# Performance work log

Measured on AMD Instinct MI355X. Metric: run time of the kernel, lower is better.

## Reference

```python
import jax, jax.numpy as jnp
import numpy as np

RADIUS = 4
SIGMA_X = 5.0
SIGMA_I = 1.0


def gaussian_kernel3d():
    # norm.pdf(d)/norm.pdf(0) == exp(-d^2/2)
    r = RADIUS
    n = 2 * r + 1
    v = np.linspace(-r, r, n) ** 2
    xy, yz, zx = np.meshgrid(v, v, v)
    dist = (xy + yz + zx) / SIGMA_X
    k = np.exp(-0.5 * dist ** 2).astype(np.float32)  # (9,9,9)
    return jnp.asarray(k)


def setup_inputs() -> dict:
    key = jax.random.key(0)
    k1, k2 = jax.random.split(key)
    B, C, K, D, H, W = 2, 1, 5, 96, 96, 96
    inputs = jax.random.normal(k1, (B, C, D, H, W), jnp.float32)
    logits = jax.random.normal(k2, (B, K, D, H, W), jnp.float32)
    labels = jax.nn.softmax(logits, axis=1)  # class probabilities
    return {"inputs": inputs, "labels": labels}


def reference(inputs, labels):
    # inputs: [B,C,D,H,W] raw image; labels: [B,K,D,H,W] class probs
    K = labels.shape[1]
    kernel = gaussian_kernel3d()
    eps_m, eps_d = 1e-5, 1e-6

    # per-class, per-channel weighted mean: [B,K,C]
    num_mean = jnp.mean(inputs[:, None] * labels[:, :, None], axis=(3, 4, 5))
    den_mean = jnp.mean(labels, axis=(2, 3, 4))[..., None] + eps_m  # [B,K,1]
    class_mean = num_mean / den_mean  # [B,K,C]

    # diff: sum over channels of (x - mean)^2 -> [B,K,D,H,W]
    diff = jnp.sum((inputs[:, None] - class_mean[..., None, None, None]) ** 2, axis=2)
    weights = jnp.exp(-(diff ** 2) / (SIGMA_I ** 2))  # [B,K,D,H,W]

    # depthwise (per-class) 3D conv with the shared Gaussian kernel
    rhs = jnp.broadcast_to(kernel[None, None], (K, 1) + kernel.shape)  # [K,1,9,9,9]
    pad = [(RADIUS, RADIUS)] * 3

    def conv(x):  # x: [B,K,D,H,W]
        return jax.lax.conv_general_dilated(
            x, rhs, window_strides=(1, 1, 1), padding=pad,
            dimension_numbers=("NCDHW", "OIDHW", "NCDHW"),
            feature_group_count=K)

    numer = jnp.sum(labels * conv(labels * weights), axis=(0, 2, 3, 4))  # [K]
    denom = jnp.sum(labels * conv(weights), axis=(0, 2, 3, 4))  # [K]
    loss = jnp.sum(jnp.abs(numer / (denom + eps_d)))  # L1Loss vs zeros per class
    return jnp.asarray(K, inputs.dtype) - loss
```

## Files before the change

kernel.cpp:

```cpp
#include <hip/hip_runtime.h>
#include <math.h>

#define VOL (96*96*96)
#define KCLS 5
#define CZ 12
#define PSTR 64
#define PROWS 40
#define PSZ (PROWS*PSTR)
#define NS2 15

typedef __attribute__((ext_vector_type(8))) short bf16x8;
typedef __attribute__((ext_vector_type(4))) float f32x4;
typedef __attribute__((ext_vector_type(4))) unsigned short us4;

constexpr int S2VALS[NS2] = {0,1,2,4,5,8,9,10,13,16,17,18,20,25,32};
constexpr int MAP33[33] = {0,1,2,-1,3,4,-1,-1,5,6,7,-1,-1,8,-1,-1,
                           9,10,11,-1,12,-1,-1,-1,-1,13,-1,-1,-1,-1,-1,-1,14};

__device__ __forceinline__ unsigned short f2bf(float f) {
  unsigned u = __builtin_bit_cast(unsigned, f);
  u += 0x7fffu + ((u >> 16) & 1u);
  return (unsigned short)(u >> 16);
}


__global__ __launch_bounds__(256) void k_sums(const float* __restrict__ I,
                                              const float* __restrict__ L,
                                              double* __restrict__ ws) {
  const int b = blockIdx.y;
  const int base = blockIdx.x * 256 + threadIdx.x;
  const float4 iv = ((const float4*)(I + b * VOL))[base];
  float sL[KCLS], sIL[KCLS];
#pragma unroll
  for (int k = 0; k < KCLS; ++k) {
    const float4 lv = ((const float4*)(L + (b * KCLS + k) * VOL))[base];
    sL[k] = (lv.x + lv.y) + (lv.z + lv.w);
    sIL[k] = iv.x * lv.x + iv.y * lv.y + iv.z * lv.z + iv.w * lv.w;
  }
#pragma unroll
  for (int k = 0; k < KCLS; ++k) {
#pragma unroll
    for (int off = 32; off; off >>= 1) {
      sL[k] += __shfl_down(sL[k], off);
      sIL[k] += __shfl_down(sIL[k], off);
    }
  }
  __shared__ double red[4][2 * KCLS];
  const int wid = threadIdx.x >> 6;
  if ((threadIdx.x & 63) == 0) {
#pragma unroll
    for (int k = 0; k < KCLS; ++k) {
      red[wid][k] = (double)sL[k];
      red[wid][KCLS + k] = (double)sIL[k];
    }
  }
  __syncthreads();
  if (threadIdx.x < 2 * KCLS) {
    double v = red[0][threadIdx.x] + red[1][threadIdx.x] + red[2][threadIdx.x] + red[3][threadIdx.x];
    const int k = threadIdx.x % KCLS;
    const int which = threadIdx.x / KCLS;
    const int slot = blockIdx.x & 31;
    atomicAdd(&ws[32 + which * 320 + (b * KCLS + k) * 32 + slot], v);
  }
}

__global__ __launch_bounds__(256, 3) void k_conv(const float* __restrict__ I,
                                                 const float* __restrict__ L,
                                                 double* __restrict__ ws) {
  __shared__ __attribute__((aligned(16))) short Wp[2][PSZ];
  __shared__ __attribute__((aligned(16))) short LWp[2][PSZ];
  __shared__ double red[8];
  __shared__ float meanS;

  const int t = threadIdx.x;
  const int vol = blockIdx.z;
  const int kcl = vol % KCLS;
  const int b = vol / KCLS;
  const int x0 = (blockIdx.x % 3) * 32;
  const int y0 = (blockIdx.x / 3) * 32;
  const int z0 = blockIdx.y * CZ;

  const float* __restrict__ Ib = I + b * VOL;
  const float* __restrict__ Lb = L + vol * VOL;

  if (t < 32) {
    double a = ws[32 + vol * 32 + t];
    double c = ws[352 + vol * 32 + t];
#pragma unroll
    for (int off = 16; off; off >>= 1) {
      a += __shfl_down(a, off);
      c += __shfl_down(c, off);
    }
    if (t == 0) meanS = (float)(c / (a + 1e-5 * (double)VOL));
  }
  __syncthreads();
  const float mean = meanS;

  const int lane = t & 63;
  const int w = t >> 6;
  const int wx = w & 1, wy = w >> 1;
  const int nn = lane & 15, qq = lane >> 4;
  const int gyOut = y0 + 16 * wy + nn;
  const int gxOut = x0 + 16 * wx + 4 * qq;

  bf16x8 afr[NS2];
#pragma unroll
  for (int r = 0; r < NS2; ++r) {
    const float s2c = (float)S2VALS[r];
    bf16x8 v;
#pragma unroll
    for (int j = 0; j < 8; ++j) {
      const int dx = 8 * qq + j - nn;
      float val = 0.f;
      if (dx >= 0 && dx <= 8) {
        const float q = s2c + (float)((dx - 4) * (dx - 4));
        val = __expf(-0.02f * q * q);
      }
      v[j] = (short)f2bf(val);
    }
    afr[r] = v;
  }

  f32x4 accW[9], accL[9];
  const f32x4 zer = {0.f, 0.f, 0.f, 0.f};
#pragma unroll
  for (int i = 0; i < 9; ++i) { accW[i] = zer; accL[i] = zer; }
  float pN = 0.f, pD = 0.f;

  auto stagePlane = [&](int buf, int zp) {
#pragma unroll
    for (int ii = 0; ii < 2; ++ii) {
      const int qi = t + ii * 256;
      if (qi < 480) {
        const int row = qi / 12;
        const int q = qi - row * 12;
        const int xq = q * 4;
        const int gy = y0 - 4 + row, gx = x0 - 4 + xq;
        const bool ok = ((unsigned)gy < 96u) && ((unsigned)gx <= 92u);
        float4 iv = make_float4(0.f, 0.f, 0.f, 0.f);
        float4 lv = make_float4(0.f, 0.f, 0.f, 0.f);
        if (ok) {
          const int off = (zp * 96 + gy) * 96 + gx;
          iv = *(const float4*)(Ib + off);
          lv = *(const float4*)(Lb + off);
        }
        float d, w0, w1, w2, w3;
        d = iv.x - mean; d = d * d; w0 = ok ? __expf(-d * d) : 0.f;
        d = iv.y - mean; d = d * d; w1 = ok ? __expf(-d * d) : 0.f;
        d = iv.z - mean; d = d * d; w2 = ok ? __expf(-d * d) : 0.f;
        d = iv.w - mean; d = d * d; w3 = ok ? __expf(-d * d) : 0.f;
        us4 wv = { f2bf(w0), f2bf(w1), f2bf(w2), f2bf(w3) };
        us4 ov = { f2bf(lv.x * w0), f2bf(lv.y * w1), f2bf(lv.z * w2), f2bf(lv.w * w3) };
        const int c = q >> 1, o = (q & 1) << 2;
        const int a = row * PSTR + (((c ^ (row & 7)) << 3) + o);
        *(us4*)(&Wp[buf][a]) = wv;
        *(us4*)(&LWp[buf][a]) = ov;
      }
    }
  };

  auto computeEdge = [&](int buf, int iLo, int iHi) {
    const short* __restrict__ Wb = Wp[buf];
    const short* __restrict__ Lwb = LWp[buf];
    const int yb = 16 * wy + nn;
    const int csel = 2 * wx + qq;
    int boff = yb * PSTR + (((csel ^ (yb & 7))) << 3);
    bf16x8 bw = *(const bf16x8*)(Wb + boff);
    bf16x8 bl = *(const bf16x8*)(Lwb + boff);
#pragma unroll
    for (int dy = 0; dy < 9; ++dy) {
      bf16x8 nbw, nbl;
      if (dy < 8) {
        const int yrow = yb + dy + 1;
        const int nboff = yrow * PSTR + (((csel ^ (yrow & 7))) << 3);
        nbw = *(const bf16x8*)(Wb + nboff);
        nbl = *(const bf16x8*)(Lwb + nboff);
      }
      const int dy2c = (dy - 4) * (dy - 4);
#pragma unroll
      for (int i = 0; i < 9; ++i) {
        if (i >= iLo && i <= iHi) {
          const int da = (i < 4) ? (4 - i) : (i - 4);
          const int ri = MAP33[dy2c + da * da];
          accW[i] = __builtin_amdgcn_mfma_f32_16x16x32_bf16(afr[ri], bw, accW[i], 0, 0, 0);
          accL[i] = __builtin_amdgcn_mfma_f32_16x16x32_bf16(afr[ri], bl, accL[i], 0, 0, 0);
        }
      }
      bw = nbw; bl = nbl;
    }
  };

  const int zp0 = z0 - 4;
  const int zend = z0 + CZ + 4;
  if ((unsigned)zp0 <= 95u) stagePlane(0, zp0);
  __syncthreads();

  for (int zp = zp0; zp < zend; ++zp) {
    const int cur = (zp - zp0) & 1;
    const int zo = zp - 4;
    const bool lok = (zo >= z0) && (zo < z0 + CZ);
    float4 lab = make_float4(0.f, 0.f, 0.f, 0.f);
    if (lok) lab = *(const float4*)(Lb + (zo * 96 + gyOut) * 96 + gxOut);

    if ((unsigned)zp <= 95u) {
      int iLo = z0 - zo; if (iLo < 0) iLo = 0;
      int iHi = (z0 + CZ - 1) - zo; if (iHi > 8) iHi = 8;
      computeEdge(cur, iLo, iHi);
    }
    if (lok) {
      pN += accL[0].x * lab.x + accL[0].y * lab.y + accL[0].z * lab.z + accL[0].w * lab.w;
      pD += accW[0].x * lab.x + accW[0].y * lab.y + accW[0].z * lab.z + accW[0].w * lab.w;
    }
#pragma unroll
    for (int i = 0; i < 8; ++i) { accW[i] = accW[i + 1]; accL[i] = accL[i + 1]; }
    accW[8] = zer; accL[8] = zer;

    const int zn = zp + 1;
    if (zn < zend && (unsigned)zn <= 95u) stagePlane(cur ^ 1, zn);
    __syncthreads();
  }

#pragma unroll
  for (int off = 32; off; off >>= 1) {
    pN += __shfl_down(pN, off);
    pD += __shfl_down(pD, off);
  }
  if (lane == 0) { red[w] = (double)pN; red[4 + w] = (double)pD; }
  __syncthreads();
  if (t == 0) {
    const int slot = (blockIdx.x + blockIdx.y) & 15;
    atomicAdd(&ws[672 + kcl * 16 + slot], red[0] + red[1] + red[2] + red[3]);
    atomicAdd(&ws[752 + kcl * 16 + slot], red[4] + red[5] + red[6] + red[7]);
  }
}

__global__ void k_final(const double* __restrict__ ws, float* __restrict__ out) {
  __shared__ double acc[KCLS];
  const int t = threadIdx.x;
  if (t < KCLS) {
    double n = 0.0, d = 0.0;
#pragma unroll
    for (int s = 0; s < 16; ++s) {
      n += ws[672 + t * 16 + s];
      d += ws[752 + t * 16 + s];
    }
    acc[t] = fabs(n / (d + 1e-6));
  }
  __syncthreads();
  if (t == 0) {
    double loss = acc[0] + acc[1] + acc[2] + acc[3] + acc[4];
    out[0] = (float)(5.0 - loss);
  }
}

extern "C" void kernel_launch(void* const* d_in, const int* in_sizes, int n_in,
                              void* d_out, int out_size, void* d_ws, size_t ws_size,
                              hipStream_t stream) {
  (void)in_sizes; (void)n_in; (void)out_size; (void)ws_size;
  const float* I = (const float*)d_in[0];
  const float* L = (const float*)d_in[1];
  double* ws = (double*)d_ws;
  float* out = (float*)d_out;

  hipMemsetAsync(d_ws, 0, 832 * sizeof(double), stream);
  k_sums<<<dim3(864, 2, 1), 256, 0, stream>>>(I, L, ws);
  k_conv<<<dim3(9, 8, 10), 256, 0, stream>>>(I, L, ws);
  k_final<<<1, 64, 0, stream>>>(ws, out);
}
```

Measured before the change: 184.4 us.

## Async LDS plane prefetch, coarsen sums kernel, fuse final reduction into conv

The conv kernel now issues global_load_lds async copies of the next raw fp32 plane into a double-buffered LDS staging area while MFMAs run on the current bf16 plane, then converts it in a separate phase. Out-of-range planes are skipped and the tail outputs are drained after the loop. The sums kernel processes four float4s per thread with a quarter of the blocks. The separate final kernel is removed, and the last conv block, detected via an atomic counter, computes the loss. LDS use rises with the raw buffers, which may lower occupancy, and there is an extra barrier per plane.

```diff
diff --git a/kernel.cpp b/kernel.cpp
--- a/kernel.cpp
+++ b/kernel.cpp
@@ -8,6 +8,7 @@
 #define PROWS 40
 #define PSZ (PROWS*PSTR)
 #define NS2 15
+#define NQ 480
 
 typedef __attribute__((ext_vector_type(8))) short bf16x8;
 typedef __attribute__((ext_vector_type(4))) float f32x4;
@@ -23,19 +24,34 @@
   return (unsigned short)(u >> 16);
 }
 
+__device__ __forceinline__ void async16(void* lds, const void* g) {
+  __builtin_amdgcn_global_load_lds(
+      (const __attribute__((address_space(1))) void*)g,
+      (__attribute__((address_space(3))) void*)lds, 16, 0, 0);
+}
+
 
 __global__ __launch_bounds__(256) void k_sums(const float* __restrict__ I,
                                               const float* __restrict__ L,
                                               double* __restrict__ ws) {
   const int b = blockIdx.y;
-  const int base = blockIdx.x * 256 + threadIdx.x;
-  const float4 iv = ((const float4*)(I + b * VOL))[base];
+  const int base = blockIdx.x * 1024 + threadIdx.x;
+  const float4* __restrict__ I4 = (const float4*)(I + b * VOL);
+  float4 iv[4];
+#pragma unroll
+  for (int j = 0; j < 4; ++j) iv[j] = I4[base + j * 256];
   float sL[KCLS], sIL[KCLS];
-#pragma unroll
+#pragma unroll 1
   for (int k = 0; k < KCLS; ++k) {
-    const float4 lv = ((const float4*)(L + (b * KCLS + k) * VOL))[base];
-    sL[k] = (lv.x + lv.y) + (lv.z + lv.w);
-    sIL[k] = iv.x * lv.x + iv.y * lv.y + iv.z * lv.z + iv.w * lv.w;
+    const float4* __restrict__ L4 = (const float4*)(L + (b * KCLS + k) * VOL);
+    float a = 0.f, c = 0.f;
+#pragma unroll
+    for (int j = 0; j < 4; ++j) {
+      const float4 lv = L4[base + j * 256];
+      a += (lv.x + lv.y) + (lv.z + lv.w);
+      c += iv[j].x * lv.x + iv[j].y * lv.y + iv[j].z * lv.z + iv[j].w * lv.w;
+    }
+    sL[k] = a; sIL[k] = c;
   }
 #pragma unroll
   for (int k = 0; k < KCLS; ++k) {
@@ -66,11 +82,15 @@
 
 __global__ __launch_bounds__(256, 3) void k_conv(const float* __restrict__ I,
                                                  const float* __restrict__ L,
-                                                 double* __restrict__ ws) {
-  __shared__ __attribute__((aligned(16))) short Wp[2][PSZ];
-  __shared__ __attribute__((aligned(16))) short LWp[2][PSZ];
+                                                 double* __restrict__ ws,
+                                                 float* __restrict__ out) {
+  __shared__ __attribute__((aligned(16))) short Wp[PSZ];
+  __shared__ __attribute__((aligned(16))) short LWp[PSZ];
+  __shared__ float4 rawI[2][NQ];
+  __shared__ float4 rawL[2][NQ];
   __shared__ double red[8];
   __shared__ float meanS;
+  __shared__ int lastS;
 
   const int t = threadIdx.x;
   const int vol = blockIdx.z;
@@ -127,23 +147,39 @@
   for (int i = 0; i < 9; ++i) { accW[i] = zer; accL[i] = zer; }
   float pN = 0.f, pD = 0.f;
 
-  auto stagePlane = [&](int buf, int zp) {
+  int qoff[2]; bool okq[2];
+#pragma unroll
+  for (int ii = 0; ii < 2; ++ii) {
+    const int qi = t + ii * 256;
+    const int row = qi / 12;
+    const int q = qi - row * 12;
+    const int gy = y0 - 4 + row, gx = x0 - 4 + q * 4;
+    okq[ii] = (qi < NQ) && ((unsigned)gy < 96u) && ((unsigned)gx <= 92u);
+    const int cy = min(max(gy, 0), 95);
+    const int cx = min(max(gx, 0), 92);
+    qoff[ii] = cy * 96 + cx;
+  }
+  const int wbase0 = t & ~63;
+  const int wbase1 = 256 + (t & ~63);
+
+  auto asyncPlane = [&](int slot, int zp) {
+    const int poff = zp * 9216;
+    async16(&rawI[slot][wbase0], Ib + poff + qoff[0]);
+    async16(&rawL[slot][wbase0], Lb + poff + qoff[0]);
+    if (t < NQ - 256) {
+      async16(&rawI[slot][wbase1], Ib + poff + qoff[1]);
+      async16(&rawL[slot][wbase1], Lb + poff + qoff[1]);
+    }
+  };
+
+  auto convertPlane = [&](int slot) {
 #pragma unroll
     for (int ii = 0; ii < 2; ++ii) {
       const int qi = t + ii * 256;
-      if (qi < 480) {
-        const int row = qi / 12;
-        const int q = qi - row * 12;
-        const int xq = q * 4;
-        const int gy = y0 - 4 + row, gx = x0 - 4 + xq;
-        const bool ok = ((unsigned)gy < 96u) && ((unsigned)gx <= 92u);
-        float4 iv = make_float4(0.f, 0.f, 0.f, 0.f);
-        float4 lv = make_float4(0.f, 0.f, 0.f, 0.f);
-        if (ok) {
-          const int off = (zp * 96 + gy) * 96 + gx;
-          iv = *(const float4*)(Ib + off);
-          lv = *(const float4*)(Lb + off);
-        }
+      if (qi < NQ) {
+        const float4 iv = rawI[slot][qi];
+        const float4 lv = rawL[slot][qi];
+        const bool ok = okq[ii];
         float d, w0, w1, w2, w3;
         d = iv.x - mean; d = d * d; w0 = ok ? __expf(-d * d) : 0.f;
         d = iv.y - mean; d = d * d; w1 = ok ? __expf(-d * d) : 0.f;
@@ -151,30 +187,30 @@
         d = iv.w - mean; d = d * d; w3 = ok ? __expf(-d * d) : 0.f;
         us4 wv = { f2bf(w0), f2bf(w1), f2bf(w2), f2bf(w3) };
         us4 ov = { f2bf(lv.x * w0), f2bf(lv.y * w1), f2bf(lv.z * w2), f2bf(lv.w * w3) };
+        const int row = qi / 12;
+        const int q = qi - row * 12;
         const int c = q >> 1, o = (q & 1) << 2;
-        const int a = row * PSTR + (((c ^ (row & 7)) << 3) + o);
-        *(us4*)(&Wp[buf][a]) = wv;
-        *(us4*)(&LWp[buf][a]) = ov;
+        const int a = row * PSTR + ((c ^ (row & 7)) << 3) + o;
+        *(us4*)(&Wp[a]) = wv;
+        *(us4*)(&LWp[a]) = ov;
       }
     }
   };
 
-  auto computeEdge = [&](int buf, int iLo, int iHi) {
-    const short* __restrict__ Wb = Wp[buf];
-    const short* __restrict__ Lwb = LWp[buf];
+  auto computeEdge = [&](int iLo, int iHi) {
     const int yb = 16 * wy + nn;
     const int csel = 2 * wx + qq;
-    int boff = yb * PSTR + (((csel ^ (yb & 7))) << 3);
-    bf16x8 bw = *(const bf16x8*)(Wb + boff);
-    bf16x8 bl = *(const bf16x8*)(Lwb + boff);
+    int boff = yb * PSTR + ((csel ^ (yb & 7)) << 3);
+    bf16x8 bw = *(const bf16x8*)(Wp + boff);
+    bf16x8 bl = *(const bf16x8*)(LWp + boff);
 #pragma unroll
     for (int dy = 0; dy < 9; ++dy) {
       bf16x8 nbw, nbl;
       if (dy < 8) {
         const int yrow = yb + dy + 1;
-        const int nboff = yrow * PSTR + (((csel ^ (yrow & 7))) << 3);
-        nbw = *(const bf16x8*)(Wb + nboff);
-        nbl = *(const bf16x8*)(Lwb + nboff);
+        const int nboff = yrow * PSTR + ((csel ^ (yrow & 7)) << 3);
+        nbw = *(const bf16x8*)(Wp + nboff);
+        nbl = *(const bf16x8*)(LWp + nboff);
       }
       const int dy2c = (dy - 4) * (dy - 4);
 #pragma unroll
@@ -190,23 +226,28 @@
     }
   };
 
-  const int zp0 = z0 - 4;
-  const int zend = z0 + CZ + 4;
-  if ((unsigned)zp0 <= 95u) stagePlane(0, zp0);
-  __syncthreads();
-
-  for (int zp = zp0; zp < zend; ++zp) {
-    const int cur = (zp - zp0) & 1;
+  const int zlo = max(z0 - 4, 0);
+  const int zhi = min(z0 + CZ + 4, 96);
+
+  asyncPlane(0, zlo);
+  __syncthreads();
+  convertPlane(0);
+  __syncthreads();
+
+  for (int zp = zlo; zp < zhi; ++zp) {
+    const int nslot = (zp + 1 - zlo) & 1;
+    const bool more = (zp + 1 < zhi);
+    if (more) asyncPlane(nslot, zp + 1);
+
     const int zo = zp - 4;
     const bool lok = (zo >= z0) && (zo < z0 + CZ);
     float4 lab = make_float4(0.f, 0.f, 0.f, 0.f);
     if (lok) lab = *(const float4*)(Lb + (zo * 96 + gyOut) * 96 + gxOut);
 
-    if ((unsigned)zp <= 95u) {
-      int iLo = z0 - zo; if (iLo < 0) iLo = 0;
-      int iHi = (z0 + CZ - 1) - zo; if (iHi > 8) iHi = 8;
-      computeEdge(cur, iLo, iHi);
-    }
+    int iLo = z0 - zo; if (iLo < 0) iLo = 0;
+    int iHi = (z0 + CZ - 1) - zo; if (iHi > 8) iHi = 8;
+    computeEdge(iLo, iHi);
+
     if (lok) {
       pN += accL[0].x * lab.x + accL[0].y * lab.y + accL[0].z * lab.z + accL[0].w * lab.w;
       pD += accW[0].x * lab.x + accW[0].y * lab.y + accW[0].z * lab.z + accW[0].w * lab.w;
@@ -215,9 +256,17 @@
     for (int i = 0; i < 8; ++i) { accW[i] = accW[i + 1]; accL[i] = accL[i + 1]; }
     accW[8] = zer; accL[8] = zer;
 
-    const int zn = zp + 1;
-    if (zn < zend && (unsigned)zn <= 95u) stagePlane(cur ^ 1, zn);
     __syncthreads();
+    if (more) convertPlane(nslot);
+    __syncthreads();
+  }
+
+  for (int zo = zhi - 4; zo < z0 + CZ; ++zo) {
+    const float4 lab = *(const float4*)(Lb + (zo * 96 + gyOut) * 96 + gxOut);
+    pN += accL[0].x * lab.x + accL[0].y * lab.y + accL[0].z * lab.z + accL[0].w * lab.w;
+    pD += accW[0].x * lab.x + accW[0].y * lab.y + accW[0].z * lab.z + accW[0].w * lab.w;
+#pragma unroll
+    for (int i = 0; i < 8; ++i) { accW[i] = accW[i + 1]; accL[i] = accL[i + 1]; }
   }
 
 #pragma unroll
@@ -231,25 +280,26 @@
     const int slot = (blockIdx.x + blockIdx.y) & 15;
     atomicAdd(&ws[672 + kcl * 16 + slot], red[0] + red[1] + red[2] + red[3]);
     atomicAdd(&ws[752 + kcl * 16 + slot], red[4] + red[5] + red[6] + red[7]);
-  }
-}
-
-__global__ void k_final(const double* __restrict__ ws, float* __restrict__ out) {
-  __shared__ double acc[KCLS];
-  const int t = threadIdx.x;
-  if (t < KCLS) {
-    double n = 0.0, d = 0.0;
-#pragma unroll
-    for (int s = 0; s < 16; ++s) {
-      n += ws[672 + t * 16 + s];
-      d += ws[752 + t * 16 + s];
-    }
-    acc[t] = fabs(n / (d + 1e-6));
-  }
-  __syncthreads();
-  if (t == 0) {
-    double loss = acc[0] + acc[1] + acc[2] + acc[3] + acc[4];
-    out[0] = (float)(5.0 - loss);
+    __threadfence();
+    const int old = atomicAdd((int*)ws, 1);
+    lastS = (old == 720 - 1);
+  }
+  __syncthreads();
+
+  if (lastS) {
+    __threadfence();
+    if (t < KCLS) {
+      double n = 0.0, d = 0.0;
+#pragma unroll
+      for (int s = 0; s < 16; ++s) {
+        n += atomicAdd(&ws[672 + t * 16 + s], 0.0);
+        d += atomicAdd(&ws[752 + t * 16 + s], 0.0);
+      }
+      red[t] = fabs(n / (d + 1e-6));
+    }
+    __syncthreads();
+    if (t == 0)
+      out[0] = (float)(5.0 - (red[0] + red[1] + red[2] + red[3] + red[4]));
   }
 }
 
@@ -263,7 +313,6 @@
   float* out = (float*)d_out;
 
   hipMemsetAsync(d_ws, 0, 832 * sizeof(double), stream);
-  k_sums<<<dim3(864, 2, 1), 256, 0, stream>>>(I, L, ws);
-  k_conv<<<dim3(9, 8, 10), 256, 0, stream>>>(I, L, ws);
-  k_final<<<1, 64, 0, stream>>>(ws, out);
-}
+  k_sums<<<dim3(216, 2, 1), 256, 0, stream>>>(I, L, ws);
+  k_conv<<<dim3(9, 8, 10), 256, 0, stream>>>(I, L, ws, out);
+}
```

Result: slower. 250.2 us (+35.7%).
